# Performance work log

Measured on AMD Instinct MI355X. Metric: run time of the kernel, lower is better.

The kernel has to match this reference:

```python
import jax, jax.numpy as jnp
import numpy as np

B, S, T = 64, 256, 256   # batch, encoder len, decoder len
U = 1024                 # num_units (LSTM, attention units, attention_layer_size)
D = 1024                 # memory feature dim
E = 1024                 # decoder embedding dim
V = 1024                 # decoder_embedding_input_dim (output Dense)


def setup_inputs() -> dict:
    key = jax.random.key(0)
    ks = jax.random.split(key, 12)
    s = 0.02
    return {
        "memory": jax.random.normal(ks[0], (B, S, D), jnp.float32),
        "dec_inputs": jax.random.normal(ks[1], (B, T, E), jnp.float32),
        "h0": jax.random.normal(ks[2], (B, U), jnp.float32),
        "c0": jax.random.normal(ks[3], (B, U), jnp.float32),
        "W_lstm": jax.random.normal(ks[4], (E + U, 4 * U), jnp.float32) * s,
        "U_lstm": jax.random.normal(ks[5], (U, 4 * U), jnp.float32) * s,
        "b_lstm": jnp.zeros((4 * U,), jnp.float32),
        "W_mem": jax.random.normal(ks[6], (D, U), jnp.float32) * s,
        "W_query": jax.random.normal(ks[7], (U, U), jnp.float32) * s,
        "v_att": jax.random.normal(ks[8], (U,), jnp.float32) * s,
        "W_attn": jax.random.normal(ks[9], (U + D, U), jnp.float32) * s,
        "W_out": jax.random.normal(ks[10], (U, V), jnp.float32) * s,
        "b_out": jnp.zeros((V,), jnp.float32),
        "mem_len": jax.random.randint(ks[11], (B,), S // 2, S + 1, jnp.int32),
    }


def reference(memory, dec_inputs, h0, c0, W_lstm, U_lstm, b_lstm,
              W_mem, W_query, v_att, W_attn, W_out, b_out, mem_len):
    # Precompute attention keys (tfa BahdanauAttention memory_layer, no bias)
    keys = jnp.einsum('bsd,du->bsu', memory, W_mem)              # [B,S,U]
    mask = jnp.arange(S)[None, :] < mem_len[:, None]             # [B,S]
    neg = jnp.asarray(-1e9, memory.dtype)

    def step(carry, x_t):
        h, c, attn = carry
        # AttentionWrapper: cell input = concat([input_t, prev_attention])
        cell_in = jnp.concatenate([x_t, attn], axis=-1)          # [B,E+U]
        z = cell_in @ W_lstm + h @ U_lstm + b_lstm               # [B,4U]
        zi, zf, zg, zo = jnp.split(z, 4, axis=-1)                # keras gate order i,f,c,o
        i = jax.nn.sigmoid(zi)
        f = jax.nn.sigmoid(zf)
        g = jnp.tanh(zg)
        o = jax.nn.sigmoid(zo)
        c_new = f * c + i * g
        h_new = o * jnp.tanh(c_new)
        # Bahdanau additive score: v^T tanh(W_q h + W_m m)
        q = h_new @ W_query                                      # [B,U]
        score = jnp.einsum('bsu,u->bs', jnp.tanh(keys + q[:, None, :]), v_att)
        score = jnp.where(mask, score, neg)
        align = jax.nn.softmax(score, axis=-1)                   # [B,S]
        context = jnp.einsum('bs,bsd->bd', align, memory)        # [B,D]
        # attention_layer (Dense(U), no bias) on concat([cell_output, context])
        attn_new = jnp.concatenate([h_new, context], axis=-1) @ W_attn  # [B,U]
        # BasicDecoder output_layer = Dense(V)
        out_t = attn_new @ W_out + b_out                         # [B,V]
        return (h_new, c_new, attn_new), out_t

    attn0 = jnp.zeros((B, U), memory.dtype)
    _, outs = jax.lax.scan(step, (h0, c0, attn0), jnp.swapaxes(dec_inputs, 0, 1))
    return jnp.swapaxes(outs, 0, 1)                              # [B,T,V]
```

## Files before the change

### kernel.cpp

```cpp
#include <hip/hip_runtime.h>

#define BB 64
#define SS 256
#define TT 256
#define UU 1024

typedef unsigned short ushort_t;
typedef __attribute__((ext_vector_type(8))) __bf16 bf16x8;
typedef __attribute__((ext_vector_type(8))) short s16x8;
typedef __attribute__((ext_vector_type(16))) float f32x16;

union PkU { s16x8 s; bf16x8 b; };

__device__ __forceinline__ ushort_t f2bf(float f) {
    unsigned u = __float_as_uint(f);
    return (ushort_t)((u + 0x7FFFu + ((u >> 16) & 1u)) >> 16);
}
__device__ __forceinline__ float bf2f(ushort_t h) {
    return __uint_as_float(((unsigned)h) << 16);
}
__device__ __forceinline__ bf16x8 ldpk(const ushort_t* p) {
    PkU u; u.s = *(const s16x8*)p; return u.b;
}
__device__ __forceinline__ void cvt8(const float* f, bf16x8& hi, bf16x8& lo) {
    PkU H, L;
#pragma unroll
    for (int e = 0; e < 8; ++e) {
        ushort_t h = f2bf(f[e]);
        H.s[e] = (short)h;
        float r = f[e] - bf2f(h);
        L.s[e] = (short)f2bf(r);
    }
    hi = H.b; lo = L.b;
}
__device__ __forceinline__ void ldcvt(const float* p, bf16x8& hi, bf16x8& lo) {
    float4 a = *(const float4*)p;
    float4 b = *(const float4*)(p + 4);
    float f[8] = {a.x, a.y, a.z, a.w, b.x, b.y, b.z, b.w};
    cvt8(f, hi, lo);
}
__device__ __forceinline__ void mfma3(f32x16& acc, bf16x8 ah, bf16x8 al, bf16x8 bh, bf16x8 bl) {
    acc = __builtin_amdgcn_mfma_f32_32x32x16_bf16(ah, bh, acc, 0, 0, 0);
    acc = __builtin_amdgcn_mfma_f32_32x32x16_bf16(ah, bl, acc, 0, 0, 0);
    acc = __builtin_amdgcn_mfma_f32_32x32x16_bf16(al, bh, acc, 0, 0, 0);
}
__device__ __forceinline__ int crow(int r, int l) {
    return (r & 3) + ((r >> 2) << 3) + ((l >> 5) << 2);
}
__device__ __forceinline__ float fast_sigmoid(float x) { return 1.f / (1.f + __expf(-x)); }
__device__ __forceinline__ float fast_tanh(float x) { return 2.f / (1.f + __expf(-2.f * x)) - 1.f; }

__global__ __launch_bounds__(256) void wsplit(
    const float* __restrict__ W, int ldw,
    ushort_t* __restrict__ pk_hi, ushort_t* __restrict__ pk_lo, int NT, int koff)
{
    __shared__ float tile[64][65];
    int k0 = blockIdx.x * 64, n0 = blockIdx.y * 64;
    int t = threadIdx.x;
    int r = t >> 2, cb = (t & 3) * 16;
    const float* src = W + (size_t)(k0 + r) * ldw + n0 + cb;
    float4 v0 = *(const float4*)(src);
    float4 v1 = *(const float4*)(src + 4);
    float4 v2 = *(const float4*)(src + 8);
    float4 v3 = *(const float4*)(src + 12);
    float vv[16] = {v0.x,v0.y,v0.z,v0.w, v1.x,v1.y,v1.z,v1.w, v2.x,v2.y,v2.z,v2.w, v3.x,v3.y,v3.z,v3.w};
#pragma unroll
    for (int i = 0; i < 16; ++i) tile[r][cb + i] = vv[i];
    __syncthreads();
#pragma unroll
    for (int i = 0; i < 2; ++i) {
        int gid = t + i * 256;
        int s_loc = gid >> 7, nt_loc = (gid >> 6) & 1, lane = gid & 63;
        int n_loc = nt_loc * 32 + (lane & 31);
        int kb = s_loc * 16 + (lane >> 5) * 8;
        float f[8];
#pragma unroll
        for (int e = 0; e < 8; ++e) f[e] = tile[kb + e][n_loc];
        bf16x8 hi, lo;
        cvt8(f, hi, lo);
        int s_glob = ((koff + k0) >> 4) + s_loc;
        int nt_glob = (n0 >> 5) + nt_loc;
        size_t off = ((size_t)(s_glob * NT + nt_glob) * 64 + lane) * 8;
        PkU H, L; H.b = hi; L.b = lo;
        *(s16x8*)(pk_hi + off) = H.s;
        *(s16x8*)(pk_lo + off) = L.s;
    }
}

__global__ __launch_bounds__(256) void pack64(
    const float* __restrict__ X, ushort_t* __restrict__ pk_hi, ushort_t* __restrict__ pk_lo)
{
    int gid = blockIdx.x * 256 + threadIdx.x;
    int lane = gid & 63, mt = (gid >> 6) & 1, s = gid >> 7;
    int r = mt * 32 + (lane & 31);
    int k = s * 16 + (lane >> 5) * 8;
    bf16x8 hi, lo;
    ldcvt(X + (size_t)r * 1024 + k, hi, lo);
    PkU H, L; H.b = hi; L.b = lo;
    size_t off = (size_t)gid * 8;
    *(s16x8*)(pk_hi + off) = H.s;
    *(s16x8*)(pk_lo + off) = L.s;
}

__global__ __launch_bounds__(256) void gemm_z(
    const float* __restrict__ dec_t, const float* __restrict__ attn_prev,
    const ushort_t* __restrict__ h_hi, const ushort_t* __restrict__ h_lo,
    const ushort_t* __restrict__ Wz_hi, const ushort_t* __restrict__ Wz_lo,
    float* __restrict__ zp)
{
    int t = threadIdx.x;
    int w = t >> 6, l = t & 63;
    int job = blockIdx.x * 4 + w;
    int ntile = job >> 3, kq = job & 7;
    int n0 = ntile * 32;
    f32x16 acc[2];
#pragma unroll
    for (int i = 0; i < 2; ++i)
#pragma unroll
        for (int r = 0; r < 16; ++r) acc[i][r] = 0.f;

#pragma unroll 2
    for (int it = 0; it < 24; ++it) {
        int kg = kq * 384 + it * 16;
        bf16x8 ah[2], al[2], bh, bl;
        int src = kg >> 10;
        if (src < 2) {
            const float* base = (src == 0) ? dec_t : attn_prev;
            int stride = (src == 0) ? (TT * 1024) : 1024;
            int kl = kg & 1023;
#pragma unroll
            for (int tm = 0; tm < 2; ++tm) {
                int row = tm * 32 + (l & 31);
                ldcvt(base + (size_t)row * stride + kl + (l >> 5) * 8, ah[tm], al[tm]);
            }
        } else {
            int sl = (kg - 2048) >> 4;
#pragma unroll
            for (int tm = 0; tm < 2; ++tm) {
                size_t off = ((size_t)(sl * 2 + tm) * 64 + l) * 8;
                ah[tm] = ldpk(h_hi + off);
                al[tm] = ldpk(h_lo + off);
            }
        }
        int s = kg >> 4;
        size_t boff = ((size_t)(s * 128 + ntile) * 64 + l) * 8;
        bh = ldpk(Wz_hi + boff);
        bl = ldpk(Wz_lo + boff);
#pragma unroll
        for (int tm = 0; tm < 2; ++tm) mfma3(acc[tm], ah[tm], al[tm], bh, bl);
    }
    float* zbase = zp + (size_t)kq * (64 * 4096);
#pragma unroll
    for (int tm = 0; tm < 2; ++tm)
#pragma unroll
        for (int r = 0; r < 16; ++r) {
            int row = tm * 32 + crow(r, l);
            int col = n0 + (l & 31);
            zbase[(size_t)row * 4096 + col] = acc[tm][r];
        }
}

__global__ __launch_bounds__(256) void gates_k(
    const float* __restrict__ zp, const float* __restrict__ b_lstm,
    const float* __restrict__ c_in, float* __restrict__ c_out,
    ushort_t* __restrict__ h_hi, ushort_t* __restrict__ h_lo)
{
    int gid = blockIdx.x * 256 + threadIdx.x;
    int b = gid >> 7, g8 = gid & 127;
    int u0 = g8 * 8;
    float zi[8], zf[8], zg[8], zo[8];
#pragma unroll
    for (int e = 0; e < 8; ++e) {
        zi[e] = b_lstm[u0 + e];
        zf[e] = b_lstm[1024 + u0 + e];
        zg[e] = b_lstm[2048 + u0 + e];
        zo[e] = b_lstm[3072 + u0 + e];
    }
    for (int kc = 0; kc < 8; ++kc) {
        const float* p = zp + (size_t)kc * 262144 + (size_t)b * 4096;
#pragma unroll
        for (int e = 0; e < 8; ++e) {
            zi[e] += p[u0 + e];
            zf[e] += p[1024 + u0 + e];
            zg[e] += p[2048 + u0 + e];
            zo[e] += p[3072 + u0 + e];
        }
    }
    float h[8], cn[8];
#pragma unroll
    for (int e = 0; e < 8; ++e) {
        float ig = fast_sigmoid(zi[e]);
        float fg = fast_sigmoid(zf[e]);
        float gg = fast_tanh(zg[e]);
        float og = fast_sigmoid(zo[e]);
        float c = fg * c_in[(size_t)b * 1024 + u0 + e] + ig * gg;
        cn[e] = c;
        h[e] = og * fast_tanh(c);
    }
#pragma unroll
    for (int e = 0; e < 8; ++e) c_out[(size_t)b * 1024 + u0 + e] = cn[e];
    bf16x8 hi, lo;
    cvt8(h, hi, lo);
    int s = u0 >> 4, mt = b >> 5;
    int lane = (b & 31) + ((u0 >> 3) & 1) * 32;
    size_t off = ((size_t)(s * 2 + mt) * 64 + lane) * 8;
    PkU H, L; H.b = hi; L.b = lo;
    *(s16x8*)(h_hi + off) = H.s;
    *(s16x8*)(h_lo + off) = L.s;
}

__global__ __launch_bounds__(256) void gemm_red(
    const ushort_t* __restrict__ A0h, const ushort_t* __restrict__ A0l,
    const ushort_t* __restrict__ A1h, const ushort_t* __restrict__ A1l,
    const ushort_t* __restrict__ Bh, const ushort_t* __restrict__ Bl,
    int Ktot, float* __restrict__ C)
{
    __shared__ float zbuf[64][33];
    int t = threadIdx.x;
    int w = t >> 6, l = t & 63;
    int bx = blockIdx.x;
    int Kc = Ktot >> 2;
    int iters = Kc >> 4;
    f32x16 acc[2];
#pragma unroll
    for (int i = 0; i < 2; ++i)
#pragma unroll
        for (int r = 0; r < 16; ++r) acc[i][r] = 0.f;

#pragma unroll 2
    for (int it = 0; it < iters; ++it) {
        int kg = w * Kc + it * 16;
        const ushort_t* ph = (kg < 1024) ? A0h : A1h;
        const ushort_t* pl = (kg < 1024) ? A0l : A1l;
        int sl = (kg & 1023) >> 4;
        bf16x8 ah[2], al[2];
#pragma unroll
        for (int tm = 0; tm < 2; ++tm) {
            size_t off = ((size_t)(sl * 2 + tm) * 64 + l) * 8;
            ah[tm] = ldpk(ph + off);
            al[tm] = ldpk(pl + off);
        }
        size_t boff = ((size_t)((kg >> 4) * 32 + bx) * 64 + l) * 8;
        bf16x8 bh = ldpk(Bh + boff);
        bf16x8 bl = ldpk(Bl + boff);
#pragma unroll
        for (int tm = 0; tm < 2; ++tm) mfma3(acc[tm], ah[tm], al[tm], bh, bl);
    }
    for (int stage = 0; stage < 4; ++stage) {
        if (w == stage) {
#pragma unroll
            for (int tm = 0; tm < 2; ++tm)
#pragma unroll
                for (int r = 0; r < 16; ++r) {
                    int row = tm * 32 + crow(r, l);
                    int col = l & 31;
                    float v = acc[tm][r];
                    if (stage == 0) zbuf[row][col] = v;
                    else zbuf[row][col] += v;
                }
        }
        __syncthreads();
    }
    int c = t & 31, bq = t >> 5;
#pragma unroll
    for (int i = 0; i < 8; ++i) {
        int b = bq * 8 + i;
        C[(size_t)b * 1024 + bx * 32 + c] = zbuf[b][c];
    }
}

template <int EPI>
__global__ __launch_bounds__(256) void gemm_span(
    const float* __restrict__ A, int lda,
    const ushort_t* __restrict__ Bh, const ushort_t* __restrict__ Bl,
    float* __restrict__ C, const float* __restrict__ bias)
{
    int t = threadIdx.x;
    int w = t >> 6, l = t & 63;
    int job = blockIdx.x * 4 + w;
    int mt = job >> 4, nt = job & 15;
    int r0 = mt * 64, n0 = nt * 64;
    f32x16 acc[4];
#pragma unroll
    for (int i = 0; i < 4; ++i)
#pragma unroll
        for (int r = 0; r < 16; ++r) acc[i][r] = 0.f;

#pragma unroll 2
    for (int it = 0; it < 64; ++it) {
        int kg = it * 16;
        bf16x8 ah[2], al[2], bh[2], bl[2];
#pragma unroll
        for (int tm = 0; tm < 2; ++tm) {
            int row = r0 + tm * 32 + (l & 31);
            ldcvt(A + (size_t)row * lda + kg + (l >> 5) * 8, ah[tm], al[tm]);
        }
#pragma unroll
        for (int tn = 0; tn < 2; ++tn) {
            size_t off = ((size_t)(it * 32 + (n0 >> 5) + tn) * 64 + l) * 8;
            bh[tn] = ldpk(Bh + off);
            bl[tn] = ldpk(Bl + off);
        }
#pragma unroll
        for (int tm = 0; tm < 2; ++tm)
#pragma unroll
            for (int tn = 0; tn < 2; ++tn)
                mfma3(acc[tm * 2 + tn], ah[tm], al[tm], bh[tn], bl[tn]);
    }
#pragma unroll
    for (int tm = 0; tm < 2; ++tm)
#pragma unroll
        for (int tn = 0; tn < 2; ++tn)
#pragma unroll
            for (int r = 0; r < 16; ++r) {
                int row = r0 + tm * 32 + crow(r, l);
                int col = n0 + tn * 32 + (l & 31);
                float v = acc[tm * 2 + tn][r];
                if (EPI == 0) {
                    C[(size_t)row * 1024 + col] = v;
                } else {
                    int tt = row >> 6, b = row & 63;
                    C[((size_t)b * 256 + tt) * 1024 + col] = v + bias[col];
                }
            }
}

__global__ __launch_bounds__(256) void scores_k(
    const float* __restrict__ keys, const float* __restrict__ q,
    const float* __restrict__ v_att, const int* __restrict__ mem_len,
    float* __restrict__ scores)
{
    __shared__ float qv[1024];
    __shared__ float vv[1024];
    int b = blockIdx.x;
    int s0 = blockIdx.y * 64;
    int tid = threadIdx.x;
    for (int e = tid; e < 1024; e += 256) {
        qv[e] = q[(size_t)b * 1024 + e];
        vv[e] = v_att[e];
    }
    __syncthreads();
    int w = tid >> 6, l = tid & 63;
    int ml = mem_len[b];
    for (int i = 0; i < 16; ++i) {
        int s = s0 + w * 16 + i;
        const float* krow = keys + ((size_t)b * SS + s) * 1024;
        float acc = 0.f;
#pragma unroll
        for (int m = 0; m < 16; ++m) {
            int u = l + m * 64;
            acc += fast_tanh(krow[u] + qv[u]) * vv[u];
        }
        for (int off = 32; off; off >>= 1) acc += __shfl_xor(acc, off);
        if (l == 0) scores[b * SS + s] = (s < ml) ? acc : -1e9f;
    }
}

__global__ __launch_bounds__(256) void ctx_k(
    const float* __restrict__ scores, const float* __restrict__ memory,
    ushort_t* __restrict__ cx_hi, ushort_t* __restrict__ cx_lo)
{
    __shared__ float al[256];
    __shared__ float red[8];
    __shared__ float ctxv[256];
    int b = blockIdx.x;
    int d0 = blockIdx.y * 256;
    int tid = threadIdx.x;

    float sc = scores[b * SS + tid];
    float m = sc;
    for (int off = 32; off; off >>= 1) m = fmaxf(m, __shfl_xor(m, off));
    if ((tid & 63) == 0) red[tid >> 6] = m;
    __syncthreads();
    m = fmaxf(fmaxf(red[0], red[1]), fmaxf(red[2], red[3]));
    float e = __expf(sc - m);
    float sum = e;
    for (int off = 32; off; off >>= 1) sum += __shfl_xor(sum, off);
    if ((tid & 63) == 0) red[4 + (tid >> 6)] = sum;
    __syncthreads();
    sum = red[4] + red[5] + red[6] + red[7];
    al[tid] = e / sum;
    __syncthreads();

    float acc = 0.f;
    int d = d0 + tid;
    const float* mrow = memory + (size_t)b * SS * 1024 + d;
#pragma unroll 4
    for (int s = 0; s < SS; ++s) acc += al[s] * mrow[(size_t)s * 1024];
    ctxv[tid] = acc;
    __syncthreads();

    if (tid < 32) {
        int d8 = d0 + tid * 8;
        float f[8];
#pragma unroll
        for (int ee = 0; ee < 8; ++ee) f[ee] = ctxv[tid * 8 + ee];
        bf16x8 hi, lo;
        cvt8(f, hi, lo);
        int s = d8 >> 4, mt = b >> 5;
        int lane = (b & 31) + ((d8 >> 3) & 1) * 32;
        size_t off = ((size_t)(s * 2 + mt) * 64 + lane) * 8;
        PkU H, L; H.b = hi; L.b = lo;
        *(s16x8*)(cx_hi + off) = H.s;
        *(s16x8*)(cx_lo + off) = L.s;
    }
}

extern "C" void kernel_launch(void* const* d_in, const int* in_sizes, int n_in,
                              void* d_out, int out_size, void* d_ws, size_t ws_size,
                              hipStream_t stream)
{
    const float* memory  = (const float*)d_in[0];
    const float* dec     = (const float*)d_in[1];
    const float* h0      = (const float*)d_in[2];
    const float* c0      = (const float*)d_in[3];
    const float* W_lstm  = (const float*)d_in[4];
    const float* U_lstm  = (const float*)d_in[5];
    const float* b_lstm  = (const float*)d_in[6];
    const float* W_mem   = (const float*)d_in[7];
    const float* W_query = (const float*)d_in[8];
    const float* v_att   = (const float*)d_in[9];
    const float* W_attn  = (const float*)d_in[10];
    const float* W_out   = (const float*)d_in[11];
    const float* b_out   = (const float*)d_in[12];
    const int*   mem_len = (const int*)d_in[13];
    float* out = (float*)d_out;

    float* ws = (float*)d_ws;
    float* keys     = ws;
    float* attn_all = keys + 16777216;
    float* zp       = attn_all + 16777216;
    float* zerob    = zp + 2097152;
    float* qbuf     = zerob + 65536;
    float* cbuf     = qbuf + 65536;
    float* scoresb  = cbuf + 65536;

    ushort_t* us    = (ushort_t*)(scoresb + 16384);
    ushort_t* Wz_hi = us;
    ushort_t* Wz_lo = Wz_hi + 12582912;
    ushort_t* Wq_hi = Wz_lo + 12582912;
    ushort_t* Wq_lo = Wq_hi + 1048576;
    ushort_t* Wa_hi = Wq_lo + 1048576;
    ushort_t* Wa_lo = Wa_hi + 2097152;
    ushort_t* Wo_hi = Wa_lo + 2097152;
    ushort_t* Wo_lo = Wo_hi + 1048576;
    ushort_t* Wm_hi = Wo_lo + 1048576;
    ushort_t* Wm_lo = Wm_hi + 1048576;
    ushort_t* h_hi  = Wm_lo + 1048576;
    ushort_t* h_lo  = h_hi + 65536;
    ushort_t* cx_hi = h_lo + 65536;
    ushort_t* cx_lo = cx_hi + 65536;

    hipMemsetAsync(zerob, 0, 65536 * sizeof(float), stream);

    wsplit<<<dim3(32, 64), 256, 0, stream>>>(W_lstm, 4096, Wz_hi, Wz_lo, 128, 0);
    wsplit<<<dim3(16, 64), 256, 0, stream>>>(U_lstm, 4096, Wz_hi, Wz_lo, 128, 2048);
    wsplit<<<dim3(16, 16), 256, 0, stream>>>(W_query, 1024, Wq_hi, Wq_lo, 32, 0);
    wsplit<<<dim3(32, 16), 256, 0, stream>>>(W_attn, 1024, Wa_hi, Wa_lo, 32, 0);
    wsplit<<<dim3(16, 16), 256, 0, stream>>>(W_out, 1024, Wo_hi, Wo_lo, 32, 0);
    wsplit<<<dim3(16, 16), 256, 0, stream>>>(W_mem, 1024, Wm_hi, Wm_lo, 32, 0);
    pack64<<<32, 256, 0, stream>>>(h0, h_hi, h_lo);

    gemm_span<0><<<1024, 256, 0, stream>>>(memory, 1024, Wm_hi, Wm_lo, keys, nullptr);

    for (int t = 0; t < TT; ++t) {
        const float* attn_prev = t ? (attn_all + (size_t)(t - 1) * 65536) : zerob;
        gemm_z<<<256, 256, 0, stream>>>(dec + (size_t)t * 1024, attn_prev,
                                        h_hi, h_lo, Wz_hi, Wz_lo, zp);
        gates_k<<<32, 256, 0, stream>>>(zp, b_lstm, t ? cbuf : c0, cbuf, h_hi, h_lo);
        gemm_red<<<32, 256, 0, stream>>>(h_hi, h_lo, h_hi, h_lo,
                                         Wq_hi, Wq_lo, 1024, qbuf);
        scores_k<<<dim3(64, 4), 256, 0, stream>>>(keys, qbuf, v_att, mem_len, scoresb);
        ctx_k<<<dim3(64, 4), 256, 0, stream>>>(scoresb, memory, cx_hi, cx_lo);
        gemm_red<<<32, 256, 0, stream>>>(h_hi, h_lo, cx_hi, cx_lo,
                                         Wa_hi, Wa_lo, 2048, attn_all + (size_t)t * 65536);
    }

    gemm_span<1><<<1024, 256, 0, stream>>>(attn_all, 1024, Wo_hi, Wo_lo, out, b_out);
}
```

Baseline: 37.73 ms.

## Fuse recurrent loop into persistent kernel with grid barriers and bf16 memory/keys

Replaces the per-timestep chain of six kernel launches with a single persistent kernel of 256 blocks that steps through all timesteps, separating the phases with atomic-counter grid barriers. Memory, keys and decoder inputs are pre-converted to bf16 packed layouts, halving the bandwidth of the score and context passes. The decoder-input part of the LSTM GEMM now uses hi-only bf16 inputs, and attention outputs are stored packed for the final output GEMM. This removes launch overhead and fp32 memory traffic at the cost of lower precision, and relies on all 256 blocks being co-resident for the barrier to avoid deadlock.

```diff
diff --git a/kernel.cpp b/kernel.cpp
--- a/kernel.cpp
+++ b/kernel.cpp
@@ -3,7 +3,6 @@
 #define BB 64
 #define SS 256
 #define TT 256
-#define UU 1024
 
 typedef unsigned short ushort_t;
 typedef __attribute__((ext_vector_type(8))) __bf16 bf16x8;
@@ -97,187 +96,48 @@
     bf16x8 hi, lo;
     ldcvt(X + (size_t)r * 1024 + k, hi, lo);
     PkU H, L; H.b = hi; L.b = lo;
-    size_t off = (size_t)gid * 8;
-    *(s16x8*)(pk_hi + off) = H.s;
-    *(s16x8*)(pk_lo + off) = L.s;
-}
-
-__global__ __launch_bounds__(256) void gemm_z(
-    const float* __restrict__ dec_t, const float* __restrict__ attn_prev,
-    const ushort_t* __restrict__ h_hi, const ushort_t* __restrict__ h_lo,
-    const ushort_t* __restrict__ Wz_hi, const ushort_t* __restrict__ Wz_lo,
-    float* __restrict__ zp)
-{
-    int t = threadIdx.x;
-    int w = t >> 6, l = t & 63;
-    int job = blockIdx.x * 4 + w;
-    int ntile = job >> 3, kq = job & 7;
-    int n0 = ntile * 32;
-    f32x16 acc[2];
-#pragma unroll
-    for (int i = 0; i < 2; ++i)
-#pragma unroll
-        for (int r = 0; r < 16; ++r) acc[i][r] = 0.f;
-
-#pragma unroll 2
-    for (int it = 0; it < 24; ++it) {
-        int kg = kq * 384 + it * 16;
-        bf16x8 ah[2], al[2], bh, bl;
-        int src = kg >> 10;
-        if (src < 2) {
-            const float* base = (src == 0) ? dec_t : attn_prev;
-            int stride = (src == 0) ? (TT * 1024) : 1024;
-            int kl = kg & 1023;
-#pragma unroll
-            for (int tm = 0; tm < 2; ++tm) {
-                int row = tm * 32 + (l & 31);
-                ldcvt(base + (size_t)row * stride + kl + (l >> 5) * 8, ah[tm], al[tm]);
-            }
-        } else {
-            int sl = (kg - 2048) >> 4;
-#pragma unroll
-            for (int tm = 0; tm < 2; ++tm) {
-                size_t off = ((size_t)(sl * 2 + tm) * 64 + l) * 8;
-                ah[tm] = ldpk(h_hi + off);
-                al[tm] = ldpk(h_lo + off);
-            }
-        }
-        int s = kg >> 4;
-        size_t boff = ((size_t)(s * 128 + ntile) * 64 + l) * 8;
-        bh = ldpk(Wz_hi + boff);
-        bl = ldpk(Wz_lo + boff);
-#pragma unroll
-        for (int tm = 0; tm < 2; ++tm) mfma3(acc[tm], ah[tm], al[tm], bh, bl);
-    }
-    float* zbase = zp + (size_t)kq * (64 * 4096);
-#pragma unroll
-    for (int tm = 0; tm < 2; ++tm)
-#pragma unroll
-        for (int r = 0; r < 16; ++r) {
-            int row = tm * 32 + crow(r, l);
-            int col = n0 + (l & 31);
-            zbase[(size_t)row * 4096 + col] = acc[tm][r];
-        }
-}
-
-__global__ __launch_bounds__(256) void gates_k(
-    const float* __restrict__ zp, const float* __restrict__ b_lstm,
-    const float* __restrict__ c_in, float* __restrict__ c_out,
-    ushort_t* __restrict__ h_hi, ushort_t* __restrict__ h_lo)
-{
-    int gid = blockIdx.x * 256 + threadIdx.x;
-    int b = gid >> 7, g8 = gid & 127;
-    int u0 = g8 * 8;
-    float zi[8], zf[8], zg[8], zo[8];
-#pragma unroll
-    for (int e = 0; e < 8; ++e) {
-        zi[e] = b_lstm[u0 + e];
-        zf[e] = b_lstm[1024 + u0 + e];
-        zg[e] = b_lstm[2048 + u0 + e];
-        zo[e] = b_lstm[3072 + u0 + e];
-    }
-    for (int kc = 0; kc < 8; ++kc) {
-        const float* p = zp + (size_t)kc * 262144 + (size_t)b * 4096;
-#pragma unroll
-        for (int e = 0; e < 8; ++e) {
-            zi[e] += p[u0 + e];
-            zf[e] += p[1024 + u0 + e];
-            zg[e] += p[2048 + u0 + e];
-            zo[e] += p[3072 + u0 + e];
-        }
-    }
-    float h[8], cn[8];
-#pragma unroll
-    for (int e = 0; e < 8; ++e) {
-        float ig = fast_sigmoid(zi[e]);
-        float fg = fast_sigmoid(zf[e]);
-        float gg = fast_tanh(zg[e]);
-        float og = fast_sigmoid(zo[e]);
-        float c = fg * c_in[(size_t)b * 1024 + u0 + e] + ig * gg;
-        cn[e] = c;
-        h[e] = og * fast_tanh(c);
-    }
-#pragma unroll
-    for (int e = 0; e < 8; ++e) c_out[(size_t)b * 1024 + u0 + e] = cn[e];
-    bf16x8 hi, lo;
-    cvt8(h, hi, lo);
-    int s = u0 >> 4, mt = b >> 5;
-    int lane = (b & 31) + ((u0 >> 3) & 1) * 32;
-    size_t off = ((size_t)(s * 2 + mt) * 64 + lane) * 8;
-    PkU H, L; H.b = hi; L.b = lo;
-    *(s16x8*)(h_hi + off) = H.s;
-    *(s16x8*)(h_lo + off) = L.s;
-}
-
-__global__ __launch_bounds__(256) void gemm_red(
-    const ushort_t* __restrict__ A0h, const ushort_t* __restrict__ A0l,
-    const ushort_t* __restrict__ A1h, const ushort_t* __restrict__ A1l,
-    const ushort_t* __restrict__ Bh, const ushort_t* __restrict__ Bl,
-    int Ktot, float* __restrict__ C)
-{
-    __shared__ float zbuf[64][33];
-    int t = threadIdx.x;
-    int w = t >> 6, l = t & 63;
-    int bx = blockIdx.x;
-    int Kc = Ktot >> 2;
-    int iters = Kc >> 4;
-    f32x16 acc[2];
-#pragma unroll
-    for (int i = 0; i < 2; ++i)
-#pragma unroll
-        for (int r = 0; r < 16; ++r) acc[i][r] = 0.f;
-
-#pragma unroll 2
-    for (int it = 0; it < iters; ++it) {
-        int kg = w * Kc + it * 16;
-        const ushort_t* ph = (kg < 1024) ? A0h : A1h;
-        const ushort_t* pl = (kg < 1024) ? A0l : A1l;
-        int sl = (kg & 1023) >> 4;
-        bf16x8 ah[2], al[2];
-#pragma unroll
-        for (int tm = 0; tm < 2; ++tm) {
-            size_t off = ((size_t)(sl * 2 + tm) * 64 + l) * 8;
-            ah[tm] = ldpk(ph + off);
-            al[tm] = ldpk(pl + off);
-        }
-        size_t boff = ((size_t)((kg >> 4) * 32 + bx) * 64 + l) * 8;
-        bf16x8 bh = ldpk(Bh + boff);
-        bf16x8 bl = ldpk(Bl + boff);
-#pragma unroll
-        for (int tm = 0; tm < 2; ++tm) mfma3(acc[tm], ah[tm], al[tm], bh, bl);
-    }
-    for (int stage = 0; stage < 4; ++stage) {
-        if (w == stage) {
-#pragma unroll
-            for (int tm = 0; tm < 2; ++tm)
-#pragma unroll
-                for (int r = 0; r < 16; ++r) {
-                    int row = tm * 32 + crow(r, l);
-                    int col = l & 31;
-                    float v = acc[tm][r];
-                    if (stage == 0) zbuf[row][col] = v;
-                    else zbuf[row][col] += v;
-                }
-        }
-        __syncthreads();
-    }
-    int c = t & 31, bq = t >> 5;
-#pragma unroll
-    for (int i = 0; i < 8; ++i) {
-        int b = bq * 8 + i;
-        C[(size_t)b * 1024 + bx * 32 + c] = zbuf[b][c];
-    }
-}
-
-template <int EPI>
-__global__ __launch_bounds__(256) void gemm_span(
-    const float* __restrict__ A, int lda,
-    const ushort_t* __restrict__ Bh, const ushort_t* __restrict__ Bl,
-    float* __restrict__ C, const float* __restrict__ bias)
-{
-    int t = threadIdx.x;
-    int w = t >> 6, l = t & 63;
-    int job = blockIdx.x * 4 + w;
+    *(s16x8*)(pk_hi + (size_t)gid * 8) = H.s;
+    *(s16x8*)(pk_lo + (size_t)gid * 8) = L.s;
+}
+
+__global__ __launch_bounds__(512) void packdec(
+    const float* __restrict__ dec, ushort_t* __restrict__ outp)
+{
+    int gid = blockIdx.x * 512 + threadIdx.x;
+    int t = gid >> 13, g = gid & 8191;
+    int s = g >> 7, mt = (g >> 6) & 1, lane = g & 63;
+    int b = mt * 32 + (lane & 31);
+    int e = s * 16 + ((lane >> 5) << 3);
+    const float* p = dec + ((size_t)b * TT + t) * 1024 + e;
+    float4 a = *(const float4*)p;
+    float4 c = *(const float4*)(p + 4);
+    float f[8] = {a.x, a.y, a.z, a.w, c.x, c.y, c.z, c.w};
+    PkU H;
+#pragma unroll
+    for (int i = 0; i < 8; ++i) H.s[i] = (short)f2bf(f[i]);
+    *(s16x8*)(outp + (size_t)gid * 8) = H.s;
+}
+
+__global__ __launch_bounds__(512) void memcvt(
+    const float* __restrict__ src, ushort_t* __restrict__ dst)
+{
+    size_t i = ((size_t)blockIdx.x * 512 + threadIdx.x) * 8;
+    float4 a = *(const float4*)(src + i);
+    float4 c = *(const float4*)(src + i + 4);
+    float f[8] = {a.x, a.y, a.z, a.w, c.x, c.y, c.z, c.w};
+    PkU H;
+#pragma unroll
+    for (int e = 0; e < 8; ++e) H.s[e] = (short)f2bf(f[e]);
+    *(s16x8*)(dst + i) = H.s;
+}
+
+__global__ __launch_bounds__(512) void gemm_keys(
+    const float* __restrict__ Amem, const ushort_t* __restrict__ Bh,
+    const ushort_t* __restrict__ Bl, ushort_t* __restrict__ keys)
+{
+    int tid = threadIdx.x;
+    int w = tid >> 6, l = tid & 63;
+    int job = blockIdx.x * 8 + w;
     int mt = job >> 4, nt = job & 15;
     int r0 = mt * 64, n0 = nt * 64;
     f32x16 acc[4];
@@ -285,21 +145,16 @@
     for (int i = 0; i < 4; ++i)
 #pragma unroll
         for (int r = 0; r < 16; ++r) acc[i][r] = 0.f;
-
-#pragma unroll 2
     for (int it = 0; it < 64; ++it) {
-        int kg = it * 16;
         bf16x8 ah[2], al[2], bh[2], bl[2];
 #pragma unroll
-        for (int tm = 0; tm < 2; ++tm) {
-            int row = r0 + tm * 32 + (l & 31);
-            ldcvt(A + (size_t)row * lda + kg + (l >> 5) * 8, ah[tm], al[tm]);
-        }
+        for (int tm = 0; tm < 2; ++tm)
+            ldcvt(Amem + (size_t)(r0 + tm * 32 + (l & 31)) * 1024 + it * 16 + (l >> 5) * 8, ah[tm], al[tm]);
 #pragma unroll
         for (int tn = 0; tn < 2; ++tn) {
-            size_t off = ((size_t)(it * 32 + (n0 >> 5) + tn) * 64 + l) * 8;
-            bh[tn] = ldpk(Bh + off);
-            bl[tn] = ldpk(Bl + off);
+            size_t boff = ((size_t)(it * 32 + nt * 2 + tn) * 64 + l) * 8;
+            bh[tn] = ldpk(Bh + boff);
+            bl[tn] = ldpk(Bl + boff);
         }
 #pragma unroll
         for (int tm = 0; tm < 2; ++tm)
@@ -315,94 +170,368 @@
             for (int r = 0; r < 16; ++r) {
                 int row = r0 + tm * 32 + crow(r, l);
                 int col = n0 + tn * 32 + (l & 31);
-                float v = acc[tm * 2 + tn][r];
-                if (EPI == 0) {
-                    C[(size_t)row * 1024 + col] = v;
+                keys[(size_t)row * 1024 + col] = f2bf(acc[tm * 2 + tn][r]);
+            }
+}
+
+__global__ __launch_bounds__(512) void gemm_out(
+    const ushort_t* __restrict__ Ah, const ushort_t* __restrict__ Al,
+    const ushort_t* __restrict__ Bh, const ushort_t* __restrict__ Bl,
+    const float* __restrict__ bias, float* __restrict__ outp)
+{
+    int tid = threadIdx.x;
+    int w = tid >> 6, l = tid & 63;
+    int job = blockIdx.x * 8 + w;
+    int t = job >> 4, nt = job & 15;
+    f32x16 acc[4];
+#pragma unroll
+    for (int i = 0; i < 4; ++i)
+#pragma unroll
+        for (int r = 0; r < 16; ++r) acc[i][r] = 0.f;
+    for (int it = 0; it < 64; ++it) {
+        bf16x8 ah[2], al[2], bh[2], bl[2];
+#pragma unroll
+        for (int tm = 0; tm < 2; ++tm) {
+            size_t g = ((size_t)t * 8192 + (size_t)it * 128 + tm * 64 + l) * 8;
+            ah[tm] = ldpk(Ah + g);
+            al[tm] = ldpk(Al + g);
+        }
+#pragma unroll
+        for (int tn = 0; tn < 2; ++tn) {
+            size_t boff = ((size_t)(it * 32 + nt * 2 + tn) * 64 + l) * 8;
+            bh[tn] = ldpk(Bh + boff);
+            bl[tn] = ldpk(Bl + boff);
+        }
+#pragma unroll
+        for (int tm = 0; tm < 2; ++tm)
+#pragma unroll
+            for (int tn = 0; tn < 2; ++tn)
+                mfma3(acc[tm * 2 + tn], ah[tm], al[tm], bh[tn], bl[tn]);
+    }
+#pragma unroll
+    for (int tm = 0; tm < 2; ++tm)
+#pragma unroll
+        for (int tn = 0; tn < 2; ++tn)
+#pragma unroll
+            for (int r = 0; r < 16; ++r) {
+                int b = tm * 32 + crow(r, l);
+                int col = nt * 64 + tn * 32 + (l & 31);
+                outp[((size_t)b * TT + t) * 1024 + col] = acc[tm * 2 + tn][r] + bias[col];
+            }
+}
+
+__device__ __forceinline__ void gridbar(unsigned* bar, unsigned target) {
+    __syncthreads();
+    if (threadIdx.x == 0) {
+        __hip_atomic_fetch_add(&bar[blockIdx.x & 7u], 1u, __ATOMIC_ACQ_REL, __HIP_MEMORY_SCOPE_AGENT);
+        if (blockIdx.x == 0) {
+            unsigned s;
+            do {
+                s = 0;
+#pragma unroll
+                for (int i = 0; i < 8; ++i)
+                    s += __hip_atomic_load(&bar[i], __ATOMIC_ACQUIRE, __HIP_MEMORY_SCOPE_AGENT);
+                if (s < target * 256u) __builtin_amdgcn_s_sleep(2);
+            } while (s < target * 256u);
+            __hip_atomic_store(&bar[8], target, __ATOMIC_RELEASE, __HIP_MEMORY_SCOPE_AGENT);
+        }
+        while (__hip_atomic_load(&bar[8], __ATOMIC_ACQUIRE, __HIP_MEMORY_SCOPE_AGENT) < target)
+            __builtin_amdgcn_s_sleep(2);
+    }
+    __syncthreads();
+}
+
+__device__ __forceinline__ void red8(float* zb, const f32x16& a0, const f32x16& a1, int w, int l) {
+    int col = l & 31;
+    if (w < 4) {
+        float* zq = zb + w * 2048;
+#pragma unroll
+        for (int r = 0; r < 16; ++r) {
+            zq[crow(r, l) * 32 + col] = a0[r];
+            zq[(32 + crow(r, l)) * 32 + col] = a1[r];
+        }
+    }
+    __syncthreads();
+    if (w >= 4) {
+        float* zq = zb + (w - 4) * 2048;
+#pragma unroll
+        for (int r = 0; r < 16; ++r) {
+            zq[crow(r, l) * 32 + col] += a0[r];
+            zq[(32 + crow(r, l)) * 32 + col] += a1[r];
+        }
+    }
+    __syncthreads();
+    if (w == 0) {
+#pragma unroll
+        for (int i = 0; i < 32; ++i) zb[i * 64 + l] += zb[2 * 2048 + i * 64 + l];
+    } else if (w == 1) {
+#pragma unroll
+        for (int i = 0; i < 32; ++i) zb[2048 + i * 64 + l] += zb[3 * 2048 + i * 64 + l];
+    }
+    __syncthreads();
+    if (w == 0) {
+#pragma unroll
+        for (int i = 0; i < 32; ++i) zb[i * 64 + l] += zb[2048 + i * 64 + l];
+    }
+    __syncthreads();
+}
+
+__global__ __launch_bounds__(512) void stepk(
+    float* __restrict__ zp, float* __restrict__ qbuf, float* __restrict__ cstate,
+    float* __restrict__ scoresb, unsigned* __restrict__ bar,
+    const ushort_t* __restrict__ Wz_hi, const ushort_t* __restrict__ Wz_lo,
+    const ushort_t* __restrict__ Wq_hi, const ushort_t* __restrict__ Wq_lo,
+    const ushort_t* __restrict__ Wa_hi, const ushort_t* __restrict__ Wa_lo,
+    const ushort_t* __restrict__ dec_pk,
+    ushort_t* __restrict__ attn_hi, ushort_t* __restrict__ attn_lo,
+    ushort_t* __restrict__ h_hi, ushort_t* __restrict__ h_lo,
+    ushort_t* __restrict__ cx_hi, ushort_t* __restrict__ cx_lo,
+    const ushort_t* __restrict__ keys, const ushort_t* __restrict__ memb,
+    const float* __restrict__ c0, const float* __restrict__ b_lstm,
+    const float* __restrict__ v_att, const int* __restrict__ mem_len)
+{
+    __shared__ float zbuf[4 * 2048];
+    __shared__ float align_s[256];
+    __shared__ float cbuf[8][128];
+    __shared__ float ctxv[256];
+    __shared__ float red[16];
+
+    const int tid = threadIdx.x;
+    const int w = tid >> 6, l = tid & 63;
+    const int bid = blockIdx.x;
+    const int nt_z = bid >> 1, kh = bid & 1;
+    unsigned ep = 0;
+
+    for (int t = 0; t < TT; ++t) {
+        {
+            f32x16 a0, a1;
+#pragma unroll
+            for (int r = 0; r < 16; ++r) { a0[r] = 0.f; a1[r] = 0.f; }
+            int sbase = kh * 96 + w * 12;
+            for (int i = 0; i < 12; ++i) {
+                int s = sbase + i;
+                size_t wo = ((size_t)(s * 128 + nt_z) * 64 + l) * 8;
+                bf16x8 bh = ldpk(Wz_hi + wo);
+                bf16x8 bl = ldpk(Wz_lo + wo);
+                if (s < 64) {
+                    const ushort_t* p = dec_pk + ((size_t)t * 8192 + (size_t)s * 128 + l) * 8;
+                    bf16x8 x0 = ldpk(p), x1 = ldpk(p + 512);
+                    a0 = __builtin_amdgcn_mfma_f32_32x32x16_bf16(x0, bh, a0, 0, 0, 0);
+                    a0 = __builtin_amdgcn_mfma_f32_32x32x16_bf16(x0, bl, a0, 0, 0, 0);
+                    a1 = __builtin_amdgcn_mfma_f32_32x32x16_bf16(x1, bh, a1, 0, 0, 0);
+                    a1 = __builtin_amdgcn_mfma_f32_32x32x16_bf16(x1, bl, a1, 0, 0, 0);
+                } else if (s < 128) {
+                    if (t) {
+                        size_t g = ((size_t)(t - 1) * 8192 + (size_t)(s - 64) * 128 + l) * 8;
+                        bf16x8 ah0 = ldpk(attn_hi + g), al0 = ldpk(attn_lo + g);
+                        bf16x8 ah1 = ldpk(attn_hi + g + 512), al1 = ldpk(attn_lo + g + 512);
+                        mfma3(a0, ah0, al0, bh, bl);
+                        mfma3(a1, ah1, al1, bh, bl);
+                    }
                 } else {
-                    int tt = row >> 6, b = row & 63;
-                    C[((size_t)b * 256 + tt) * 1024 + col] = v + bias[col];
+                    size_t g = ((size_t)(s - 128) * 128 + l) * 8;
+                    bf16x8 hh0 = ldpk(h_hi + g), hl0 = ldpk(h_lo + g);
+                    bf16x8 hh1 = ldpk(h_hi + g + 512), hl1 = ldpk(h_lo + g + 512);
+                    mfma3(a0, hh0, hl0, bh, bl);
+                    mfma3(a1, hh1, hl1, bh, bl);
                 }
             }
-}
-
-__global__ __launch_bounds__(256) void scores_k(
-    const float* __restrict__ keys, const float* __restrict__ q,
-    const float* __restrict__ v_att, const int* __restrict__ mem_len,
-    float* __restrict__ scores)
-{
-    __shared__ float qv[1024];
-    __shared__ float vv[1024];
-    int b = blockIdx.x;
-    int s0 = blockIdx.y * 64;
-    int tid = threadIdx.x;
-    for (int e = tid; e < 1024; e += 256) {
-        qv[e] = q[(size_t)b * 1024 + e];
-        vv[e] = v_att[e];
-    }
-    __syncthreads();
-    int w = tid >> 6, l = tid & 63;
-    int ml = mem_len[b];
-    for (int i = 0; i < 16; ++i) {
-        int s = s0 + w * 16 + i;
-        const float* krow = keys + ((size_t)b * SS + s) * 1024;
-        float acc = 0.f;
-#pragma unroll
-        for (int m = 0; m < 16; ++m) {
-            int u = l + m * 64;
-            acc += fast_tanh(krow[u] + qv[u]) * vv[u];
-        }
-        for (int off = 32; off; off >>= 1) acc += __shfl_xor(acc, off);
-        if (l == 0) scores[b * SS + s] = (s < ml) ? acc : -1e9f;
-    }
-}
-
-__global__ __launch_bounds__(256) void ctx_k(
-    const float* __restrict__ scores, const float* __restrict__ memory,
-    ushort_t* __restrict__ cx_hi, ushort_t* __restrict__ cx_lo)
-{
-    __shared__ float al[256];
-    __shared__ float red[8];
-    __shared__ float ctxv[256];
-    int b = blockIdx.x;
-    int d0 = blockIdx.y * 256;
-    int tid = threadIdx.x;
-
-    float sc = scores[b * SS + tid];
-    float m = sc;
-    for (int off = 32; off; off >>= 1) m = fmaxf(m, __shfl_xor(m, off));
-    if ((tid & 63) == 0) red[tid >> 6] = m;
-    __syncthreads();
-    m = fmaxf(fmaxf(red[0], red[1]), fmaxf(red[2], red[3]));
-    float e = __expf(sc - m);
-    float sum = e;
-    for (int off = 32; off; off >>= 1) sum += __shfl_xor(sum, off);
-    if ((tid & 63) == 0) red[4 + (tid >> 6)] = sum;
-    __syncthreads();
-    sum = red[4] + red[5] + red[6] + red[7];
-    al[tid] = e / sum;
-    __syncthreads();
-
-    float acc = 0.f;
-    int d = d0 + tid;
-    const float* mrow = memory + (size_t)b * SS * 1024 + d;
-#pragma unroll 4
-    for (int s = 0; s < SS; ++s) acc += al[s] * mrow[(size_t)s * 1024];
-    ctxv[tid] = acc;
-    __syncthreads();
-
-    if (tid < 32) {
-        int d8 = d0 + tid * 8;
-        float f[8];
-#pragma unroll
-        for (int ee = 0; ee < 8; ++ee) f[ee] = ctxv[tid * 8 + ee];
-        bf16x8 hi, lo;
-        cvt8(f, hi, lo);
-        int s = d8 >> 4, mt = b >> 5;
-        int lane = (b & 31) + ((d8 >> 3) & 1) * 32;
-        size_t off = ((size_t)(s * 2 + mt) * 64 + lane) * 8;
-        PkU H, L; H.b = hi; L.b = lo;
-        *(s16x8*)(cx_hi + off) = H.s;
-        *(s16x8*)(cx_lo + off) = L.s;
+            red8(zbuf, a0, a1, w, l);
+            float* zpk = zp + (size_t)kh * 262144;
+#pragma unroll
+            for (int i = 0; i < 4; ++i) {
+                int el = tid + i * 512;
+                zpk[(size_t)(el >> 5) * 4096 + nt_z * 32 + (el & 31)] = zbuf[el];
+            }
+        }
+        gridbar(bar, ++ep);
+
+        if (tid < 32) {
+            int g = bid * 32 + tid;
+            int s = g >> 7, mt = (g >> 6) & 1, lane = g & 63;
+            int b = mt * 32 + (lane & 31);
+            int u0 = s * 16 + ((lane >> 5) << 3);
+            float zz[4][8];
+#pragma unroll
+            for (int gg = 0; gg < 4; ++gg) {
+                float4 b0 = *(const float4*)(b_lstm + gg * 1024 + u0);
+                float4 b1 = *(const float4*)(b_lstm + gg * 1024 + u0 + 4);
+                zz[gg][0] = b0.x; zz[gg][1] = b0.y; zz[gg][2] = b0.z; zz[gg][3] = b0.w;
+                zz[gg][4] = b1.x; zz[gg][5] = b1.y; zz[gg][6] = b1.z; zz[gg][7] = b1.w;
+#pragma unroll
+                for (int k2 = 0; k2 < 2; ++k2) {
+                    const float* p = zp + (size_t)k2 * 262144 + (size_t)b * 4096 + gg * 1024 + u0;
+                    float4 x0 = *(const float4*)p;
+                    float4 x1 = *(const float4*)(p + 4);
+                    zz[gg][0] += x0.x; zz[gg][1] += x0.y; zz[gg][2] += x0.z; zz[gg][3] += x0.w;
+                    zz[gg][4] += x1.x; zz[gg][5] += x1.y; zz[gg][6] += x1.z; zz[gg][7] += x1.w;
+                }
+            }
+            const float* cin = t ? cstate : c0;
+            float hv[8];
+#pragma unroll
+            for (int e = 0; e < 8; ++e) {
+                float ig = fast_sigmoid(zz[0][e]);
+                float fg = fast_sigmoid(zz[1][e]);
+                float gg_ = fast_tanh(zz[2][e]);
+                float og = fast_sigmoid(zz[3][e]);
+                float c = fg * cin[(size_t)b * 1024 + u0 + e] + ig * gg_;
+                cstate[(size_t)b * 1024 + u0 + e] = c;
+                hv[e] = og * fast_tanh(c);
+            }
+            bf16x8 hi, lo;
+            cvt8(hv, hi, lo);
+            PkU H, L; H.b = hi; L.b = lo;
+            *(s16x8*)(h_hi + (size_t)g * 8) = H.s;
+            *(s16x8*)(h_lo + (size_t)g * 8) = L.s;
+        }
+        gridbar(bar, ++ep);
+
+        if (bid < 32) {
+            f32x16 a0, a1;
+#pragma unroll
+            for (int r = 0; r < 16; ++r) { a0[r] = 0.f; a1[r] = 0.f; }
+            for (int i = 0; i < 8; ++i) {
+                int s = w * 8 + i;
+                size_t g = ((size_t)s * 128 + l) * 8;
+                bf16x8 hh0 = ldpk(h_hi + g), hl0 = ldpk(h_lo + g);
+                bf16x8 hh1 = ldpk(h_hi + g + 512), hl1 = ldpk(h_lo + g + 512);
+                size_t boff = ((size_t)(s * 32 + bid) * 64 + l) * 8;
+                bf16x8 bh = ldpk(Wq_hi + boff), bl = ldpk(Wq_lo + boff);
+                mfma3(a0, hh0, hl0, bh, bl);
+                mfma3(a1, hh1, hl1, bh, bl);
+            }
+            red8(zbuf, a0, a1, w, l);
+#pragma unroll
+            for (int i = 0; i < 4; ++i) {
+                int el = tid + i * 512;
+                qbuf[(size_t)(el >> 5) * 1024 + bid * 32 + (el & 31)] = zbuf[el];
+            }
+        }
+        gridbar(bar, ++ep);
+
+        {
+            int job = bid * 8 + w;
+            int b = job >> 5, sblk = job & 31;
+            float qv[16], vv[16];
+#pragma unroll
+            for (int i = 0; i < 4; ++i) {
+                float4 q4 = *(const float4*)(qbuf + (size_t)b * 1024 + l * 16 + i * 4);
+                float4 v4 = *(const float4*)(v_att + l * 16 + i * 4);
+                qv[i*4] = q4.x; qv[i*4+1] = q4.y; qv[i*4+2] = q4.z; qv[i*4+3] = q4.w;
+                vv[i*4] = v4.x; vv[i*4+1] = v4.y; vv[i*4+2] = v4.z; vv[i*4+3] = v4.w;
+            }
+            int ml = mem_len[b];
+            for (int rr = 0; rr < 8; ++rr) {
+                int s = sblk * 8 + rr;
+                const ushort_t* kp = keys + ((size_t)(b * SS + s) * 1024) + l * 16;
+                s16x8 k0 = *(const s16x8*)kp;
+                s16x8 k1 = *(const s16x8*)(kp + 8);
+                float acc = 0.f;
+#pragma unroll
+                for (int e = 0; e < 8; ++e)
+                    acc += fast_tanh(bf2f((ushort_t)k0[e]) + qv[e]) * vv[e];
+#pragma unroll
+                for (int e = 0; e < 8; ++e)
+                    acc += fast_tanh(bf2f((ushort_t)k1[e]) + qv[8 + e]) * vv[8 + e];
+#pragma unroll
+                for (int off = 32; off; off >>= 1) acc += __shfl_xor(acc, off);
+                if (l == 0) scoresb[b * SS + s] = (s < ml) ? acc : -1e9f;
+            }
+        }
+        gridbar(bar, ++ep);
+
+        {
+            int b = bid >> 2, dpair = bid & 3;
+            int ss = tid & 255;
+            float sc = scoresb[b * SS + ss];
+            float m = sc;
+#pragma unroll
+            for (int off = 32; off; off >>= 1) m = fmaxf(m, __shfl_xor(m, off));
+            if (l == 0) red[w] = m;
+            __syncthreads();
+            m = fmaxf(fmaxf(fmaxf(red[0], red[1]), fmaxf(red[2], red[3])),
+                      fmaxf(fmaxf(red[4], red[5]), fmaxf(red[6], red[7])));
+            float e = __expf(sc - m);
+            if (tid < 256) align_s[ss] = e;
+            float su = e;
+#pragma unroll
+            for (int off = 32; off; off >>= 1) su += __shfl_xor(su, off);
+            if (l == 0) red[8 + w] = su;
+            __syncthreads();
+            float rinv = 1.f / (red[8] + red[9] + red[10] + red[11]);
+            int dchunk = dpair * 2 + (w >> 2), sq = w & 3;
+            int d0 = dchunk * 128 + l * 2;
+            float c0a = 0.f, c1a = 0.f;
+            for (int i = 0; i < 64; ++i) {
+                int s = sq * 64 + i;
+                float al = align_s[s];
+                unsigned mv = *(const unsigned*)(memb + ((size_t)(b * SS + s) * 1024) + d0);
+                c0a += al * bf2f((ushort_t)(mv & 0xffffu));
+                c1a += al * bf2f((ushort_t)(mv >> 16));
+            }
+            cbuf[w][l * 2] = c0a;
+            cbuf[w][l * 2 + 1] = c1a;
+            __syncthreads();
+            if (tid < 256) {
+                int dc = tid >> 7, idx = tid & 127;
+                ctxv[tid] = (cbuf[dc * 4][idx] + cbuf[dc * 4 + 1][idx] +
+                             cbuf[dc * 4 + 2][idx] + cbuf[dc * 4 + 3][idx]) * rinv;
+            }
+            __syncthreads();
+            if (tid < 32) {
+                float f[8];
+#pragma unroll
+                for (int e2 = 0; e2 < 8; ++e2) f[e2] = ctxv[tid * 8 + e2];
+                bf16x8 hi, lo;
+                cvt8(f, hi, lo);
+                int dg = dpair * 256 + tid * 8;
+                int sg = dg >> 4, hih = (dg >> 3) & 1;
+                int laneg = (hih << 5) + (b & 31);
+                int mtg = b >> 5;
+                size_t g = ((size_t)sg * 128 + mtg * 64 + laneg) * 8;
+                PkU H, L; H.b = hi; L.b = lo;
+                *(s16x8*)(cx_hi + g) = H.s;
+                *(s16x8*)(cx_lo + g) = L.s;
+            }
+        }
+        gridbar(bar, ++ep);
+
+        if (bid < 32) {
+            f32x16 a0, a1;
+#pragma unroll
+            for (int r = 0; r < 16; ++r) { a0[r] = 0.f; a1[r] = 0.f; }
+            for (int i = 0; i < 16; ++i) {
+                int s = w * 16 + i;
+                const ushort_t* ph = (s < 64) ? h_hi : cx_hi;
+                const ushort_t* pl = (s < 64) ? h_lo : cx_lo;
+                int sl = s & 63;
+                size_t g = ((size_t)sl * 128 + l) * 8;
+                bf16x8 x0h = ldpk(ph + g), x0l = ldpk(pl + g);
+                bf16x8 x1h = ldpk(ph + g + 512), x1l = ldpk(pl + g + 512);
+                size_t boff = ((size_t)(s * 32 + bid) * 64 + l) * 8;
+                bf16x8 bh = ldpk(Wa_hi + boff), bl = ldpk(Wa_lo + boff);
+                mfma3(a0, x0h, x0l, bh, bl);
+                mfma3(a1, x1h, x1l, bh, bl);
+            }
+            red8(zbuf, a0, a1, w, l);
+            if (tid < 256) {
+                int sl_loc = tid >> 7, mtg = (tid >> 6) & 1, laneg = tid & 63;
+                int b = mtg * 32 + (laneg & 31);
+                int lc = sl_loc * 16 + ((laneg >> 5) << 3);
+                float f[8];
+#pragma unroll
+                for (int e2 = 0; e2 < 8; ++e2) f[e2] = zbuf[b * 32 + lc + e2];
+                bf16x8 hi, lo;
+                cvt8(f, hi, lo);
+                int sg = bid * 2 + sl_loc;
+                size_t g = ((size_t)t * 8192 + (size_t)sg * 128 + mtg * 64 + laneg) * 8;
+                PkU H, L; H.b = hi; L.b = lo;
+                *(s16x8*)(attn_hi + g) = H.s;
+                *(s16x8*)(attn_lo + g) = L.s;
+            }
+        }
+        gridbar(bar, ++ep);
     }
 }
 
@@ -427,15 +556,13 @@
     float* out = (float*)d_out;
 
     float* ws = (float*)d_ws;
-    float* keys     = ws;
-    float* attn_all = keys + 16777216;
-    float* zp       = attn_all + 16777216;
-    float* zerob    = zp + 2097152;
-    float* qbuf     = zerob + 65536;
-    float* cbuf     = qbuf + 65536;
-    float* scoresb  = cbuf + 65536;
-
-    ushort_t* us    = (ushort_t*)(scoresb + 16384);
+    float* zp      = ws;
+    float* qbuf    = zp + 524288;
+    float* cstate  = qbuf + 65536;
+    float* scoresb = cstate + 65536;
+    unsigned* bar  = (unsigned*)(scoresb + 16384);
+
+    ushort_t* us    = (ushort_t*)(bar + 16);
     ushort_t* Wz_hi = us;
     ushort_t* Wz_lo = Wz_hi + 12582912;
     ushort_t* Wq_hi = Wz_lo + 12582912;
@@ -446,12 +573,17 @@
     ushort_t* Wo_lo = Wo_hi + 1048576;
     ushort_t* Wm_hi = Wo_lo + 1048576;
     ushort_t* Wm_lo = Wm_hi + 1048576;
-    ushort_t* h_hi  = Wm_lo + 1048576;
+    ushort_t* dec_pk  = Wm_lo + 1048576;
+    ushort_t* attn_hi = dec_pk + 16777216;
+    ushort_t* attn_lo = attn_hi + 16777216;
+    ushort_t* h_hi  = attn_lo + 16777216;
     ushort_t* h_lo  = h_hi + 65536;
     ushort_t* cx_hi = h_lo + 65536;
     ushort_t* cx_lo = cx_hi + 65536;
-
-    hipMemsetAsync(zerob, 0, 65536 * sizeof(float), stream);
+    ushort_t* keysb = cx_lo + 65536;
+    ushort_t* memb  = keysb + 16777216;
+
+    hipMemsetAsync(bar, 0, 64, stream);
 
     wsplit<<<dim3(32, 64), 256, 0, stream>>>(W_lstm, 4096, Wz_hi, Wz_lo, 128, 0);
     wsplit<<<dim3(16, 64), 256, 0, stream>>>(U_lstm, 4096, Wz_hi, Wz_lo, 128, 2048);
@@ -460,21 +592,15 @@
     wsplit<<<dim3(16, 16), 256, 0, stream>>>(W_out, 1024, Wo_hi, Wo_lo, 32, 0);
     wsplit<<<dim3(16, 16), 256, 0, stream>>>(W_mem, 1024, Wm_hi, Wm_lo, 32, 0);
     pack64<<<32, 256, 0, stream>>>(h0, h_hi, h_lo);
-
-    gemm_span<0><<<1024, 256, 0, stream>>>(memory, 1024, Wm_hi, Wm_lo, keys, nullptr);
-
-    for (int t = 0; t < TT; ++t) {
-        const float* attn_prev = t ? (attn_all + (size_t)(t - 1) * 65536) : zerob;
-        gemm_z<<<256, 256, 0, stream>>>(dec + (size_t)t * 1024, attn_prev,
-                                        h_hi, h_lo, Wz_hi, Wz_lo, zp);
-        gates_k<<<32, 256, 0, stream>>>(zp, b_lstm, t ? cbuf : c0, cbuf, h_hi, h_lo);
-        gemm_red<<<32, 256, 0, stream>>>(h_hi, h_lo, h_hi, h_lo,
-                                         Wq_hi, Wq_lo, 1024, qbuf);
-        scores_k<<<dim3(64, 4), 256, 0, stream>>>(keys, qbuf, v_att, mem_len, scoresb);
-        ctx_k<<<dim3(64, 4), 256, 0, stream>>>(scoresb, memory, cx_hi, cx_lo);
-        gemm_red<<<32, 256, 0, stream>>>(h_hi, h_lo, cx_hi, cx_lo,
-                                         Wa_hi, Wa_lo, 2048, attn_all + (size_t)t * 65536);
-    }
-
-    gemm_span<1><<<1024, 256, 0, stream>>>(attn_all, 1024, Wo_hi, Wo_lo, out, b_out);
-}
+    packdec<<<4096, 512, 0, stream>>>(dec, dec_pk);
+    memcvt<<<4096, 512, 0, stream>>>(memory, memb);
+    gemm_keys<<<512, 512, 0, stream>>>(memory, Wm_hi, Wm_lo, keysb);
+
+    stepk<<<256, 512, 0, stream>>>(
+        zp, qbuf, cstate, scoresb, bar,
+        Wz_hi, Wz_lo, Wq_hi, Wq_lo, Wa_hi, Wa_lo,
+        dec_pk, attn_hi, attn_lo, h_hi, h_lo, cx_hi, cx_lo,
+        keysb, memb, c0, b_lstm, v_att, mem_len);
+
+    gemm_out<<<512, 512, 0, stream>>>(attn_hi, attn_lo, Wo_hi, Wo_lo, b_out, out);
+}
```

New measurement: 102.0 ms. 2.7x slower.
